# Kernel optimization log

Hardware: AMD Instinct MI355X
Metric: run time of the kernel (lower is better)

## Reference

```python
import jax, jax.numpy as jnp
import numpy as np

# 8-bit signed symmetric quantization grid (bit buffer in the module is set to 8 at runtime)
SAT_MAX = 127.0
SAT_MIN = -127.0


def _squant_stage(rn, re, un, ue, up_p, dn, de, dn_p):
    """One SQuant flip stage over the last axis (vectorized SQuant_func).

    For each row: e = sum(rounding_error); flip round(|e|) elements.
    If e < 0 (under-rounded overall) flip the highest-up-priority elements up,
    else flip the highest-down-priority elements down. The boundary (last,
    lowest-priority flipped) element gets a nonzero priority in the opposite
    direction so the next (coarser) stage can revert it — this reproduces the
    in-place priority update SQuant_func performs after zeroing priorities.
    All tensors have shape [..., K].
    """
    e_sum = jnp.sum(re, axis=-1)                                   # [...]
    n_flip = jnp.round(jnp.abs(e_sum)).astype(jnp.int32)[..., None]  # [...,1]
    flip_up = (e_sum < 0)[..., None]                               # [...,1]
    prio = jnp.where(flip_up, up_p, dn_p)
    order = jnp.argsort(-prio, axis=-1)        # descending priority
    rank = jnp.argsort(order, axis=-1)         # rank[i] = position of i in order
    mask = rank < n_flip                       # elements to flip
    rn2 = jnp.where(mask, jnp.where(flip_up, un, dn), rn)
    re2 = jnp.where(mask, jnp.where(flip_up, ue, de), re)
    # boundary element (rank == n_flip-1) gets opposite-direction priority
    boundary = mask & (rank == (n_flip - 1))
    b_prio = jnp.where(boundary, jnp.abs(re2), 0.0)
    up_p2 = jnp.where(flip_up, jnp.zeros_like(b_prio), b_prio)
    dn_p2 = jnp.where(flip_up, b_prio, jnp.zeros_like(b_prio))
    return rn2, re2, up_p2, dn_p2


def adaptive_round(x, t_min, t_max):
    rn = jnp.round(x)
    re = rn - x
    # up candidates: elements rounded down (re < 0) and not saturated high
    ue = jnp.where((x >= t_max) | (re > 0), 0.0, re)
    up_p = jnp.abs(ue)
    nz_u = ue != 0
    ue = jnp.where(nz_u, ue + 1.0, ue)
    un = jnp.where(nz_u, rn + 1.0, rn)
    # down candidates: elements rounded up (re > 0) and not saturated low
    de = jnp.where((x <= t_min) | (re < 0), 0.0, re)
    dn_p = jnp.abs(de)
    nz_d = de != 0
    de = jnp.where(nz_d, de - 1.0, de)
    dn = jnp.where(nz_d, rn - 1.0, rn)

    OC, IC = x.shape[0], x.shape[1]
    K = x.size // (OC * IC)
    shp_k = (OC, IC, K)         # squant-k: per (oc, ic) kernel row
    rn_k, re_k, up_p_k, dn_p_k = _squant_stage(
        rn.reshape(shp_k), re.reshape(shp_k),
        un.reshape(shp_k), ue.reshape(shp_k), up_p.reshape(shp_k),
        dn.reshape(shp_k), de.reshape(shp_k), dn_p.reshape(shp_k))
    shp_c = (1, OC, IC * K)     # squant-c: per oc channel row
    rn_c, _, _, _ = _squant_stage(
        rn_k.reshape(shp_c), re_k.reshape(shp_c),
        un.reshape(shp_c), ue.reshape(shp_c), up_p_k.reshape(shp_c),
        dn.reshape(shp_c), de.reshape(shp_c), dn_p_k.reshape(shp_c))
    return rn_c.reshape(x.shape)


def setup_inputs() -> dict:
    key = jax.random.key(0)
    tensor = jax.random.normal(key, (1024, 1024, 3, 3), dtype=jnp.float32)
    return {"tensor": tensor}


def reference(tensor) -> jnp.ndarray:
    # symmetric linear quantization params from tensor min/max (weight path)
    max_abs = jnp.maximum(jnp.abs(jnp.max(tensor)), jnp.abs(jnp.min(tensor)))
    scale = max_abs / SAT_MAX                       # element scale
    q = jnp.clip(tensor / scale, SAT_MIN, SAT_MAX)  # linear_quantize
    q = adaptive_round(q, SAT_MIN, SAT_MAX)         # SQuant adaptive rounding
    return q * scale                                # linear_dequantize
```

## Files before the change

### kernel.cpp

```cpp
#include <hip/hip_runtime.h>

#define OC 1024
#define ICN 1024
#define KK 9
#define NELEM (OC * ICN * KK)
#define CH (ICN * KK)
#define CH4 (CH / 4)
#define BT 512
#define KMB 1024

__global__ void __launch_bounds__(256) kmax_part(const float* __restrict__ x,
                                                 float* __restrict__ part) {
    __shared__ float s_m[4];
    const int tid = blockIdx.x * 256 + threadIdx.x;
    const int stride = KMB * 256;
    const float4* x4 = (const float4*)x;
    float m = 0.f;
    #pragma unroll
    for (int k = 0; k < 9; ++k) {
        float4 v = x4[tid + k * stride];
        m = fmaxf(m, fmaxf(fmaxf(fabsf(v.x), fabsf(v.y)), fmaxf(fabsf(v.z), fabsf(v.w))));
    }
    #pragma unroll
    for (int off = 32; off > 0; off >>= 1)
        m = fmaxf(m, __shfl_xor(m, off, 64));
    if ((threadIdx.x & 63) == 0) s_m[threadIdx.x >> 6] = m;
    __syncthreads();
    if (threadIdx.x == 0)
        part[blockIdx.x] = fmaxf(fmaxf(s_m[0], s_m[1]), fmaxf(s_m[2], s_m[3]));
}

__global__ void __launch_bounds__(256) kmax_atomic(const float* __restrict__ x,
                                                   unsigned* __restrict__ ws) {
    __shared__ float s_m[4];
    const int tid = blockIdx.x * 256 + threadIdx.x;
    const int stride = KMB * 256;
    const float4* x4 = (const float4*)x;
    float m = 0.f;
    #pragma unroll
    for (int k = 0; k < 9; ++k) {
        float4 v = x4[tid + k * stride];
        m = fmaxf(m, fmaxf(fmaxf(fabsf(v.x), fabsf(v.y)), fmaxf(fabsf(v.z), fabsf(v.w))));
    }
    #pragma unroll
    for (int off = 32; off > 0; off >>= 1)
        m = fmaxf(m, __shfl_xor(m, off, 64));
    if ((threadIdx.x & 63) == 0) s_m[threadIdx.x >> 6] = m;
    __syncthreads();
    if (threadIdx.x == 0) {
        m = fmaxf(fmaxf(s_m[0], s_m[1]), fmaxf(s_m[2], s_m[3]));
        atomicMax(ws, __float_as_uint(m));
    }
}

template <int C>
__device__ __forceinline__ unsigned dpp_add_step(unsigned v) {
    unsigned o = (unsigned)__builtin_amdgcn_update_dpp(0, (int)v, C, 0xF, 0xF, false);
    return v + o;
}
__device__ __forceinline__ unsigned wave_sum_u32(unsigned v) {
    v = dpp_add_step<0x111>(v);
    v = dpp_add_step<0x112>(v);
    v = dpp_add_step<0x114>(v);
    v = dpp_add_step<0x118>(v);
    v = dpp_add_step<0x142>(v);
    v = dpp_add_step<0x143>(v);
    return (unsigned)__builtin_amdgcn_readlane((int)v, 63);
}

__global__ void __launch_bounds__(BT, 8) squant_kernel(const float* __restrict__ x,
                                                       float* __restrict__ out,
                                                       const float* __restrict__ part,
                                                       int nparts) {
    __shared__ __align__(16) signed char s_q[CH];
    __shared__ float s_res[ICN];
    __shared__ float s_prio[ICN];
    __shared__ int   s_meta[ICN];

    const int oc = blockIdx.x;
    const int t  = threadIdx.x;
    const long long ocbase = (long long)oc * CH;

    const float* p0 = x + ocbase + (long long)t * KK;
    const float* p1 = p0 + (long long)BT * KK;
    float a0[KK], a1[KK];
    #pragma unroll
    for (int k = 0; k < KK; ++k) a0[k] = p0[k];
    #pragma unroll
    for (int k = 0; k < KK; ++k) a1[k] = p1[k];

    float m;
    if (nparts > 0) {
        m = 0.f;
        #pragma unroll
        for (int i = 0; i < 16; ++i) m = fmaxf(m, part[(t & 63) + i * 64]);
        #pragma unroll
        for (int off = 32; off > 0; off >>= 1)
            m = fmaxf(m, __shfl_xor(m, off, 64));
    } else {
        m = __uint_as_float(((const unsigned*)part)[0]);
    }
    const float scale = m / 127.0f;
    const float iscale = 1.0f / scale;

    #pragma unroll
    for (int half = 0; half < 2; ++half) {
        const int row = t + half * BT;
        float rn[KK], re[KK];
        float e = 0.f;
        #pragma unroll
        for (int k = 0; k < KK; ++k) {
            float q = (half ? a1[k] : a0[k]) * iscale;
            q = fminf(fmaxf(q, -127.f), 127.f);
            float r = rintf(q);
            rn[k] = r;
            re[k] = r - q;
            e += re[k];
        }
        int nf = (int)rintf(fabsf(e));
        bool up = e < 0.f;
        unsigned flipped = 0u;
        int bidx = -1;
        float b_re = 0.f;
        for (int f = 0; f < nf; ++f) {
            float bp = 0.f; int bk = -1; float cre = 0.f;
            #pragma unroll
            for (int k = 0; k < KK; ++k) {
                bool cand = up ? (re[k] < 0.f) : (re[k] > 0.f);
                float p = (cand && !((flipped >> k) & 1u)) ? fabsf(re[k]) : 0.f;
                if (p > bp) { bp = p; bk = k; cre = re[k]; }
            }
            if (bk < 0) break;
            flipped |= (1u << bk);
            bidx = bk; b_re = cre;
        }
        int cnt = __popc(flipped);
        float sgn = up ? 1.f : -1.f;

        float* po = out + ocbase + (long long)row * KK;
        #pragma unroll
        for (int k = 0; k < KK; ++k) {
            float v = rn[k] + (((flipped >> k) & 1u) ? sgn : 0.f);
            po[k] = v * scale;
            s_q[row * KK + k] = (signed char)(int)v;
        }
        s_res[row] = e + sgn * (float)cnt;
        if (bidx >= 0) {
            s_prio[row] = fabsf(b_re + sgn);
            s_meta[row] = (row * KK + bidx) | ((up ? 1 : 0) << 16);
        } else {
            s_prio[row] = 0.f;
            s_meta[row] = 0;
        }
    }
    __syncthreads();

    if (t < 64) {
        float s = 0.f;
        #pragma unroll
        for (int i = 0; i < ICN / 64; ++i) s += s_res[t + i * 64];
        #pragma unroll
        for (int off = 32; off > 0; off >>= 1) s += __shfl_xor(s, off, 64);

        int n2 = (int)rintf(fabsf(s));
        bool up2 = s < 0.f;
        if (n2 > 0) {
            unsigned k[ICN / 64];
            #pragma unroll
            for (int i = 0; i < ICN / 64; ++i) {
                int r = t + i * 64;
                float pr = s_prio[r];
                int dir = s_meta[r] >> 16;
                bool match = ((dir != 0) != up2);
                unsigned bits = __float_as_uint(pr);
                k[i] = (pr > 0.f && match)
                         ? (((bits - 0x3F000000u + 1u) << 4) | (15u - (unsigned)i))
                         : 0u;
            }

            unsigned cloc = 0u;
            #pragma unroll
            for (int i = 0; i < ICN / 64; ++i) cloc += (k[i] != 0u) ? 1u : 0u;
            unsigned Ctot = wave_sum_u32(cloc);

            int f = 0;
            if (Ctot > 0u) {
                unsigned nsel = ((unsigned)n2 < Ctot) ? (unsigned)n2 : Ctot;

                unsigned T = 0u;
                for (int b = 27; b >= 0; --b) {
                    unsigned cand = T | (1u << b);
                    unsigned c = 0u;
                    #pragma unroll
                    for (int i = 0; i < ICN / 64; ++i) c += (k[i] >= cand) ? 1u : 0u;
                    if (wave_sum_u32(c) >= nsel) T = cand;
                }

                unsigned c1loc = 0u;
                unsigned fmask = 0u;
                #pragma unroll
                for (int i = 0; i < ICN / 64; ++i) {
                    if (k[i] > T) { fmask |= (1u << i); c1loc += 1u; }
                }
                unsigned C1 = wave_sum_u32(c1loc);
                int need = (int)nsel - (int)C1;

                int tie_i = -1;
                #pragma unroll
                for (int i = 0; i < ICN / 64; ++i) {
                    if (k[i] == T) tie_i = i;
                }
                unsigned long long tmask = __ballot(tie_i >= 0);
                int rank = __popcll(tmask & ((1ull << t) - 1ull));
                if (tie_i >= 0 && rank < need) fmask |= (1u << tie_i);

                f = (int)nsel;

                #pragma unroll
                for (int i = 0; i < ICN / 64; ++i) {
                    if ((fmask >> i) & 1u) {
                        int meta = s_meta[t + i * 64];
                        int gid = meta & 0xFFFF;
                        int nq = (int)s_q[gid] + ((meta >> 16) ? -1 : 1);
                        out[ocbase + gid] = (float)nq * scale;
                    }
                }
            }

            if (f < n2) {
                int remaining = n2 - f;
                if (remaining > CH) remaining = CH;
                for (int j = t; j < remaining; j += 64) {
                    float q = x[ocbase + j] * iscale;
                    q = fminf(fmaxf(q, -127.f), 127.f);
                    float r = rintf(q);
                    float rr = r - q;
                    float v = up2 ? ((rr < 0.f) ? r + 1.f : r)
                                  : ((rr > 0.f) ? r - 1.f : r);
                    out[ocbase + j] = v * scale;
                }
            }
        }
    }
}

extern "C" void kernel_launch(void* const* d_in, const int* in_sizes, int n_in,
                              void* d_out, int out_size, void* d_ws, size_t ws_size,
                              hipStream_t stream) {
    const float* x = (const float*)d_in[0];
    float* out = (float*)d_out;
    if (ws_size >= KMB * sizeof(float)) {
        float* part = (float*)d_ws;
        kmax_part<<<KMB, 256, 0, stream>>>(x, part);
        squant_kernel<<<OC, BT, 0, stream>>>(x, out, part, KMB);
    } else {
        unsigned* wsmax = (unsigned*)d_ws;
        hipMemsetAsync(d_ws, 0, 4, stream);
        kmax_atomic<<<KMB, 256, 0, stream>>>(x, wsmax);
        squant_kernel<<<OC, BT, 0, stream>>>(x, out, (const float*)d_ws, 0);
    }
}
```

Before: 103.4 us.

## Split squant into streaming quant kernel and per-channel fixup kernel via workspace

Adds a new path that, when the workspace is large enough, splits the fused squant kernel into two kernels. The first streams all elements, does the per-kernel flip stage and writes output directly, along with per-row residual, boundary priority and metadata in global memory. The second is a small one-wave-per-channel kernel that does the channel-level selection and patches a few outputs. The aim is to keep the bandwidth-heavy pass free of the serial wave-level selection and its shared-memory footprint, so occupancy and streaming improve. The cost is an extra launch and a read-back of the modified output values. It also relies on the harness providing about 12 MB of workspace.

```diff
diff --git a/kernel.cpp b/kernel.cpp
--- a/kernel.cpp
+++ b/kernel.cpp
@@ -8,6 +8,8 @@
 #define CH4 (CH / 4)
 #define BT 512
 #define KMB 1024
+#define NROWS (OC * ICN)
+#define WS_NEED (4096 + 3 * NROWS * 4)
 
 __global__ void __launch_bounds__(256) kmax_part(const float* __restrict__ x,
                                                  float* __restrict__ part) {
@@ -68,6 +70,191 @@
     return (unsigned)__builtin_amdgcn_readlane((int)v, 63);
 }
 
+__device__ __forceinline__ float scale_from_part(const float* __restrict__ part, int t) {
+    float m = 0.f;
+    #pragma unroll
+    for (int i = 0; i < 16; ++i) m = fmaxf(m, part[(t & 63) + i * 64]);
+    #pragma unroll
+    for (int off = 32; off > 0; off >>= 1)
+        m = fmaxf(m, __shfl_xor(m, off, 64));
+    return m / 127.0f;
+}
+
+__global__ void __launch_bounds__(BT, 8) quant_stream(const float* __restrict__ x,
+                                                      float* __restrict__ out,
+                                                      const float* __restrict__ part,
+                                                      float* __restrict__ g_res,
+                                                      float* __restrict__ g_prio,
+                                                      int* __restrict__ g_meta) {
+    const int oc = blockIdx.x;
+    const int t  = threadIdx.x;
+    const long long ocbase = (long long)oc * CH;
+    const int rowbase = oc * ICN;
+
+    const float* p0 = x + ocbase + (long long)t * KK;
+    const float* p1 = p0 + (long long)BT * KK;
+    float a0[KK], a1[KK];
+    #pragma unroll
+    for (int k = 0; k < KK; ++k) a0[k] = p0[k];
+    #pragma unroll
+    for (int k = 0; k < KK; ++k) a1[k] = p1[k];
+
+    const float scale = scale_from_part(part, t);
+    const float iscale = 1.0f / scale;
+
+    #pragma unroll
+    for (int half = 0; half < 2; ++half) {
+        const int row = t + half * BT;
+        float rn[KK], re[KK];
+        float e = 0.f;
+        #pragma unroll
+        for (int k = 0; k < KK; ++k) {
+            float q = (half ? a1[k] : a0[k]) * iscale;
+            q = fminf(fmaxf(q, -127.f), 127.f);
+            float r = rintf(q);
+            rn[k] = r;
+            re[k] = r - q;
+            e += re[k];
+        }
+        int nf = (int)rintf(fabsf(e));
+        bool up = e < 0.f;
+        unsigned flipped = 0u;
+        int bidx = -1;
+        float b_re = 0.f;
+        for (int f = 0; f < nf; ++f) {
+            float bp = 0.f; int bk = -1; float cre = 0.f;
+            #pragma unroll
+            for (int k = 0; k < KK; ++k) {
+                bool cand = up ? (re[k] < 0.f) : (re[k] > 0.f);
+                float p = (cand && !((flipped >> k) & 1u)) ? fabsf(re[k]) : 0.f;
+                if (p > bp) { bp = p; bk = k; cre = re[k]; }
+            }
+            if (bk < 0) break;
+            flipped |= (1u << bk);
+            bidx = bk; b_re = cre;
+        }
+        int cnt = __popc(flipped);
+        float sgn = up ? 1.f : -1.f;
+
+        float* po = out + ocbase + (long long)row * KK;
+        #pragma unroll
+        for (int k = 0; k < KK; ++k) {
+            float v = rn[k] + (((flipped >> k) & 1u) ? sgn : 0.f);
+            po[k] = v * scale;
+        }
+        g_res[rowbase + row] = e + sgn * (float)cnt;
+        if (bidx >= 0) {
+            g_prio[rowbase + row] = fabsf(b_re + sgn);
+            g_meta[rowbase + row] = (row * KK + bidx) | ((up ? 1 : 0) << 16);
+        } else {
+            g_prio[rowbase + row] = 0.f;
+            g_meta[rowbase + row] = 0;
+        }
+    }
+}
+
+__global__ void __launch_bounds__(64) fixup_kernel(const float* __restrict__ x,
+                                                   float* __restrict__ out,
+                                                   const float* __restrict__ part,
+                                                   const float* __restrict__ g_res,
+                                                   const float* __restrict__ g_prio,
+                                                   const int* __restrict__ g_meta) {
+    const int oc = blockIdx.x;
+    const int t  = threadIdx.x;
+    const long long ocbase = (long long)oc * CH;
+    const int rowbase = oc * ICN;
+
+    const float scale = scale_from_part(part, t);
+    const float iscale = 1.0f / scale;
+
+    float s = 0.f;
+    #pragma unroll
+    for (int i = 0; i < ICN / 64; ++i) s += g_res[rowbase + t + i * 64];
+    #pragma unroll
+    for (int off = 32; off > 0; off >>= 1) s += __shfl_xor(s, off, 64);
+
+    int n2 = (int)rintf(fabsf(s));
+    bool up2 = s < 0.f;
+    if (n2 == 0) return;
+
+    unsigned k[ICN / 64];
+    #pragma unroll
+    for (int i = 0; i < ICN / 64; ++i) {
+        int r = rowbase + t + i * 64;
+        float pr = g_prio[r];
+        int dir = g_meta[r] >> 16;
+        bool match = ((dir != 0) != up2);
+        unsigned bits = __float_as_uint(pr);
+        k[i] = (pr > 0.f && match)
+                 ? (((bits - 0x3F000000u + 1u) << 4) | (15u - (unsigned)i))
+                 : 0u;
+    }
+
+    unsigned cloc = 0u;
+    #pragma unroll
+    for (int i = 0; i < ICN / 64; ++i) cloc += (k[i] != 0u) ? 1u : 0u;
+    unsigned Ctot = wave_sum_u32(cloc);
+
+    int f = 0;
+    if (Ctot > 0u) {
+        unsigned nsel = ((unsigned)n2 < Ctot) ? (unsigned)n2 : Ctot;
+
+        unsigned T = 0u;
+        for (int b = 27; b >= 0; --b) {
+            unsigned cand = T | (1u << b);
+            unsigned c = 0u;
+            #pragma unroll
+            for (int i = 0; i < ICN / 64; ++i) c += (k[i] >= cand) ? 1u : 0u;
+            if (wave_sum_u32(c) >= nsel) T = cand;
+        }
+
+        unsigned c1loc = 0u;
+        unsigned fmask = 0u;
+        #pragma unroll
+        for (int i = 0; i < ICN / 64; ++i) {
+            if (k[i] > T) { fmask |= (1u << i); c1loc += 1u; }
+        }
+        unsigned C1 = wave_sum_u32(c1loc);
+        int need = (int)nsel - (int)C1;
+
+        int tie_i = -1;
+        #pragma unroll
+        for (int i = 0; i < ICN / 64; ++i) {
+            if (k[i] == T) tie_i = i;
+        }
+        unsigned long long tmask = __ballot(tie_i >= 0);
+        int rank = __popcll(tmask & ((1ull << t) - 1ull));
+        if (tie_i >= 0 && rank < need) fmask |= (1u << tie_i);
+
+        f = (int)nsel;
+
+        #pragma unroll
+        for (int i = 0; i < ICN / 64; ++i) {
+            if ((fmask >> i) & 1u) {
+                int meta = g_meta[rowbase + t + i * 64];
+                int gid = meta & 0xFFFF;
+                float qv = rintf(out[ocbase + gid] * iscale);
+                float nq = qv + ((meta >> 16) ? -1.f : 1.f);
+                out[ocbase + gid] = nq * scale;
+            }
+        }
+    }
+
+    if (f < n2) {
+        int remaining = n2 - f;
+        if (remaining > CH) remaining = CH;
+        for (int j = t; j < remaining; j += 64) {
+            float q = x[ocbase + j] * iscale;
+            q = fminf(fmaxf(q, -127.f), 127.f);
+            float r = rintf(q);
+            float rr = r - q;
+            float v = up2 ? ((rr < 0.f) ? r + 1.f : r)
+                          : ((rr > 0.f) ? r - 1.f : r);
+            out[ocbase + j] = v * scale;
+        }
+    }
+}
+
 __global__ void __launch_bounds__(BT, 8) squant_kernel(const float* __restrict__ x,
                                                        float* __restrict__ out,
                                                        const float* __restrict__ part,
@@ -91,12 +278,7 @@
 
     float m;
     if (nparts > 0) {
-        m = 0.f;
-        #pragma unroll
-        for (int i = 0; i < 16; ++i) m = fmaxf(m, part[(t & 63) + i * 64]);
-        #pragma unroll
-        for (int off = 32; off > 0; off >>= 1)
-            m = fmaxf(m, __shfl_xor(m, off, 64));
+        m = scale_from_part(part, t) * 127.0f;
     } else {
         m = __uint_as_float(((const unsigned*)part)[0]);
     }
@@ -177,7 +359,6 @@
                          ? (((bits - 0x3F000000u + 1u) << 4) | (15u - (unsigned)i))
                          : 0u;
             }
-
             unsigned cloc = 0u;
             #pragma unroll
             for (int i = 0; i < ICN / 64; ++i) cloc += (k[i] != 0u) ? 1u : 0u;
@@ -186,7 +367,6 @@
             int f = 0;
             if (Ctot > 0u) {
                 unsigned nsel = ((unsigned)n2 < Ctot) ? (unsigned)n2 : Ctot;
-
                 unsigned T = 0u;
                 for (int b = 27; b >= 0; --b) {
                     unsigned cand = T | (1u << b);
@@ -195,7 +375,6 @@
                     for (int i = 0; i < ICN / 64; ++i) c += (k[i] >= cand) ? 1u : 0u;
                     if (wave_sum_u32(c) >= nsel) T = cand;
                 }
-
                 unsigned c1loc = 0u;
                 unsigned fmask = 0u;
                 #pragma unroll
@@ -204,7 +383,6 @@
                 }
                 unsigned C1 = wave_sum_u32(c1loc);
                 int need = (int)nsel - (int)C1;
-
                 int tie_i = -1;
                 #pragma unroll
                 for (int i = 0; i < ICN / 64; ++i) {
@@ -213,9 +391,7 @@
                 unsigned long long tmask = __ballot(tie_i >= 0);
                 int rank = __popcll(tmask & ((1ull << t) - 1ull));
                 if (tie_i >= 0 && rank < need) fmask |= (1u << tie_i);
-
                 f = (int)nsel;
-
                 #pragma unroll
                 for (int i = 0; i < ICN / 64; ++i) {
                     if ((fmask >> i) & 1u) {
@@ -226,7 +402,6 @@
                     }
                 }
             }
-
             if (f < n2) {
                 int remaining = n2 - f;
                 if (remaining > CH) remaining = CH;
@@ -249,7 +424,15 @@
                               hipStream_t stream) {
     const float* x = (const float*)d_in[0];
     float* out = (float*)d_out;
-    if (ws_size >= KMB * sizeof(float)) {
+    if (ws_size >= (size_t)WS_NEED) {
+        float* part  = (float*)d_ws;
+        float* g_res = (float*)((char*)d_ws + 4096);
+        float* g_prio = g_res + NROWS;
+        int*   g_meta = (int*)(g_prio + NROWS);
+        kmax_part<<<KMB, 256, 0, stream>>>(x, part);
+        quant_stream<<<OC, BT, 0, stream>>>(x, out, part, g_res, g_prio, g_meta);
+        fixup_kernel<<<OC, 64, 0, stream>>>(x, out, part, g_res, g_prio, g_meta);
+    } else if (ws_size >= KMB * sizeof(float)) {
         float* part = (float*)d_ws;
         kmax_part<<<KMB, 256, 0, stream>>>(x, part);
         squant_kernel<<<OC, BT, 0, stream>>>(x, out, part, KMB);
```

Result: slower. 110.9 us (+7.2%).
